# Performance work log

Hardware: AMD Instinct MI355X
Metric: run time of the kernel (lower is better)

The kernel has to match this reference:

```python
import jax, jax.numpy as jnp
import numpy as np

V_PATCH = (1, 2, 4, 8, 16, 32)
RESI = 0.5   # abs(quant_resi)
BETA = 0.25
K_PHI = 4    # share_quant_resi


def _phi_idx(si, SN, K=K_PHI):
    # PhiPartiallyShared.__getitem__ with at = si/(SN-1)
    ticks = np.linspace(1/3/K, 1 - 1/3/K, K) if K == 4 else np.linspace(1/2/K, 1 - 1/2/K, K)
    return int(np.argmin(np.abs(ticks - si / (SN - 1))))


def _area_down(x, pn):
    # F.interpolate mode='area' with pn | H  == exact block mean
    B, C, H, W = x.shape
    return x.reshape(B, C, pn, H // pn, pn, W // pn).mean(axis=(3, 5))


def _bilinear(x, size):
    # matches torch bilinear, align_corners=False, antialias=False (half-pixel centers)
    B, C, _, _ = x.shape
    return jax.image.resize(x, (B, C, size, size), method='bilinear', antialias=False)


def _down(x, pn, si):
    if pn == x.shape[2]:
        return x
    return _area_down(x, pn) if si <= 3 else _bilinear(x, pn)


def _phi_ada(h, w, b, fw, fb, sn):
    # Phi_ada: conv weight modulated by fc(SN); fc is zero-init but kept in the graph
    C = h.shape[1]
    cond = (fw[:, 0] * jnp.float32(sn) + fb).reshape(C, C, 1, 1)
    wmod = w * (1.0 + cond)
    y = jax.lax.conv_general_dilated(h, wmod, (1, 1), 'SAME',
                                     dimension_numbers=('NCHW', 'OIHW', 'NCHW'))
    y = y + b[None, :, None, None]
    return h * (1.0 - RESI) + y * RESI


def _forward(f, embed_w, conv_w, conv_b, fc_w, fc_b):
    B, C, H, W = f.shape
    SN = len(V_PATCH)
    f_ng = jax.lax.stop_gradient(f)
    f_rest = f_ng
    f_hat = jnp.zeros_like(f_ng)
    e_ng = jax.lax.stop_gradient(embed_w)            # embedding.weight.data
    e_sq = jnp.sum(e_ng * e_ng, axis=1)              # [V]
    vq_losses = []
    commit = jnp.float32(0.0)
    for si, pn in enumerate(V_PATCH):
        rest = f_rest if si == SN - 1 else _down(f_rest, pn, si)
        rest_NC = rest.transpose(0, 2, 3, 1).reshape(-1, C)          # [N,C]
        # squared L2 distances to codebook, argmin (non-differentiable)
        d = (jnp.sum(rest_NC * rest_NC, axis=1, keepdims=True)
             + e_sq - 2.0 * (rest_NC @ e_ng.T))                       # [N,V]
        idx = jnp.argmin(d, axis=1)                                   # [N]
        h = embed_w[idx].reshape(B, pn, pn, C).transpose(0, 3, 1, 2)  # [B,C,pn,pn]
        if si != SN - 1:
            h = _bilinear(h, H)
        k = _phi_idx(si, SN)
        h = _phi_ada(h, conv_w[k], conv_b[k], fc_w[k], fc_b[k], SN)
        f_hat = f_hat + h
        f_rest = f_rest - jax.lax.stop_gradient(h)    # grad through f_rest is killed by argmin anyway
        vq_losses.append(jnp.mean((f_hat - f_ng) ** 2))
        fh_ng = jax.lax.stop_gradient(f_hat)
        commit = commit + jnp.mean((_down(fh_ng, pn, si) - _down(f, pn, si)) ** 2) * BETA
    commit = commit / SN
    # straight-through estimator
    f_hat_out = jax.lax.stop_gradient(f_hat) - f_ng + f
    return f_hat_out, jnp.stack(vq_losses), commit


def setup_inputs() -> dict:
    key = jax.random.key(0)
    k1, k2, k3 = jax.random.split(key, 3)
    B, C, H, W = 32, 64, 32, 32
    V = 4096
    f_BChw = jax.random.normal(k1, (B, C, H, W), dtype=jnp.float32)
    embed_w = jax.random.normal(k2, (V, C), dtype=jnp.float32) * 0.5  # trunc_normal std=0.5
    conv_w = jax.random.normal(k3, (K_PHI, C, C, 3, 3), dtype=jnp.float32) * 0.02
    conv_b = jnp.zeros((K_PHI, C), dtype=jnp.float32)
    fc_w = jnp.zeros((K_PHI, C * C, 1), dtype=jnp.float32)  # Phi_ada.fc zero-init
    fc_b = jnp.zeros((K_PHI, C * C), dtype=jnp.float32)
    return {'f_BChw': f_BChw, 'embed_w': embed_w, 'conv_w': conv_w,
            'conv_b': conv_b, 'fc_w': fc_w, 'fc_b': fc_b}


def reference(f_BChw, embed_w, conv_w, conv_b, fc_w, fc_b):
    return _forward(f_BChw, embed_w, conv_w, conv_b, fc_w, fc_b)
```

## Files before the change

### kernel.cpp

```cpp
#include <hip/hip_runtime.h>
#include <cfloat>

#define N_ELEM 2097152
#define TAU 2.0e-2f

typedef short s16x8 __attribute__((ext_vector_type(8)));
typedef float f32x4 __attribute__((ext_vector_type(4)));

__device__ __forceinline__ unsigned short f2bf(float v) {
    unsigned u = __float_as_uint(v);
    u += 0x7FFFu + ((u >> 16) & 1u);
    return (unsigned short)(u >> 16);
}
__device__ __forceinline__ float bf2f(unsigned short h) {
    return __uint_as_float(((unsigned)h) << 16);
}

__device__ __forceinline__ float blockReduceSum(float v) {
    __shared__ float red[4];
    #pragma unroll
    for (int off = 32; off; off >>= 1) v += __shfl_down(v, off, 64);
    int wid = threadIdx.x >> 6, lane = threadIdx.x & 63;
    if (lane == 0) red[wid] = v;
    __syncthreads();
    float r = 0.f;
    if (threadIdx.x == 0) {
        int nw = ((int)blockDim.x + 63) >> 6;
        for (int w = 0; w < nw; ++w) r += red[w];
    }
    __syncthreads();
    return r;
}

__global__ void k_embprep(const float* __restrict__ e, float* __restrict__ hesq,
                          unsigned short* __restrict__ ehiN, unsigned short* __restrict__ eloN) {
    int v = blockIdx.x * 256 + threadIdx.x;
    if (v >= 4096) return;
    const float4* r = (const float4*)(e + (size_t)v * 64);
    float s = 0.f;
    #pragma unroll
    for (int i = 0; i < 16; ++i) {
        float4 a = r[i];
        s += a.x * a.x + a.y * a.y + a.z * a.z + a.w * a.w;
    }
    hesq[v] = 0.5f * s;
    for (int i = 0; i < 64; ++i) {
        float x = e[(size_t)v * 64 + i];
        unsigned short h = f2bf(x);
        ehiN[(size_t)v * 64 + i] = h ^ 0x8000u;
        eloN[(size_t)v * 64 + i] = f2bf(x - bf2f(h)) ^ 0x8000u;
    }
}

__global__ void k_wmod(const float* __restrict__ w, const float* __restrict__ fcw,
                       const float* __restrict__ fcb,
                       unsigned short* __restrict__ wh, unsigned short* __restrict__ wl) {
    int i = blockIdx.x * 256 + threadIdx.x;
    if (i >= 4 * 64 * 64 * 9) return;
    int k = i / (64 * 64 * 9);
    int r = i % (64 * 64 * 9);
    int oi = r / 9;
    int t = r % 9;
    int co = oi >> 6, ci = oi & 63;
    float cond = fcw[k * 4096 + oi] * 6.0f + fcb[k * 4096 + oi];
    float v = w[i] * (1.0f + cond);
    size_t o = ((size_t)(k * 9 + t) * 64 + co) * 64 + ci;
    unsigned short h = f2bf(v);
    wh[o] = h;
    wl[o] = f2bf(v - bf2f(h));
}

__global__ __launch_bounds__(256) void k_down_plane(
        const float* __restrict__ f, const float* __restrict__ fhat,
        float* __restrict__ restnc, unsigned short* __restrict__ dhi,
        unsigned short* __restrict__ dlo, float* __restrict__ cmpPrev, int pn) {
    __shared__ float hs[32][16];
    __shared__ float cr[32][16];
    __shared__ float pm[256];
    int bc = blockIdx.x;
    int c = bc & 63, b = bc >> 6;
    int t = threadIdx.x;
    const float4* fp = (const float4*)(f + (size_t)bc * 1024);
    const float4* hp = (const float4*)(fhat + (size_t)bc * 1024);
    float4 a = fp[t], q = hp[t];
    int r = t >> 3, c4 = t & 7;
    hs[r][c4 * 2]     = (a.x - q.x) + (a.y - q.y);
    hs[r][c4 * 2 + 1] = (a.z - q.z) + (a.w - q.w);
    __syncthreads();
    int cpp = 16 / pn;
    for (int i = t; i < 32 * pn; i += 256) {
        int rr = i / pn, px = i % pn;
        float s = 0.f;
        for (int j = 0; j < cpp; ++j) s += hs[rr][px * cpp + j];
        cr[rr][px] = s;
    }
    __syncthreads();
    int s_ = 32 / pn;
    float inv = 1.0f / (float)(s_ * s_);
    for (int p = t; p < pn * pn; p += 256) {
        int py = p / pn, px = p % pn;
        float s = 0.f;
        for (int j = 0; j < s_; ++j) s += cr[py * s_ + j][px];
        float m = s * inv;
        pm[p] = m;
        int n = (b * pn + py) * pn + px;
        size_t o = (size_t)n * 64 + c;
        unsigned short h = f2bf(m);
        restnc[o] = m;
        dhi[o] = h;
        dlo[o] = f2bf(m - bf2f(h));
    }
    if (pn >= 2) {
        __syncthreads();
        int pnp = pn >> 1;
        float m2 = 0.f;
        for (int p = t; p < pnp * pnp; p += 256) {
            int py = p / pnp, px = p % pnp;
            float mm = 0.25f * (pm[(2 * py) * pn + 2 * px] + pm[(2 * py) * pn + 2 * px + 1]
                              + pm[(2 * py + 1) * pn + 2 * px] + pm[(2 * py + 1) * pn + 2 * px + 1]);
            m2 += mm * mm;
        }
        m2 = blockReduceSum(m2);
        if (t == 0) cmpPrev[blockIdx.x] = m2;
    }
}

__global__ void k_trans_nc(const float* __restrict__ A, const float* __restrict__ Bt,
                           float* __restrict__ dst,
                           unsigned short* __restrict__ dhi, unsigned short* __restrict__ dlo) {
    __shared__ float t[64][65];
    int b = blockIdx.x;
    int p0 = blockIdx.y * 64;
    int lane = threadIdx.x & 63, r4 = threadIdx.x >> 6;
    #pragma unroll
    for (int i = 0; i < 16; ++i) {
        int c = i * 4 + r4;
        size_t g = ((size_t)b * 64 + c) * 1024 + p0 + lane;
        t[c][lane] = A[g] - Bt[g];
    }
    __syncthreads();
    #pragma unroll
    for (int i = 0; i < 16; ++i) {
        int p = i * 4 + r4;
        size_t o = ((size_t)(b * 1024 + p0 + p)) * 64 + lane;
        float v = t[lane][p];
        unsigned short h = f2bf(v);
        dst[o] = v;
        dhi[o] = h;
        dlo[o] = f2bf(v - bf2f(h));
    }
}

__global__ __launch_bounds__(256) void k_commit_rest(const float* __restrict__ restnc,
                                                     float* __restrict__ cmp) {
    int i = blockIdx.x * 256 + threadIdx.x;
    int c = i & 63;
    int p = i >> 6;
    int px = p & 15; p >>= 4;
    int py = p & 15; p >>= 4;
    int b = p;
    int n00 = (b * 32 + 2 * py) * 32 + 2 * px;
    float m = 0.25f * (restnc[(size_t)n00 * 64 + c] + restnc[(size_t)(n00 + 1) * 64 + c]
                     + restnc[(size_t)(n00 + 32) * 64 + c] + restnc[(size_t)(n00 + 33) * 64 + c]);
    float m2 = blockReduceSum(m * m);
    if (threadIdx.x == 0) cmp[blockIdx.x] = m2;
}

__global__ __launch_bounds__(256) void k_vq_mfma(
        const unsigned short* __restrict__ resthi, const unsigned short* __restrict__ restlo,
        const unsigned short* __restrict__ embhiN, const unsigned short* __restrict__ embloN,
        const float* __restrict__ hesq,
        float* __restrict__ m1v_, int* __restrict__ m1i_, float* __restrict__ m2v_,
        int N, int CPS) {
    __shared__ __align__(16) unsigned short lah[64 * 64];
    __shared__ __align__(16) unsigned short lal[64 * 64];
    __shared__ __align__(16) float lq[64];
    int tid = threadIdx.x;
    int lane = tid & 63, wv = tid >> 6;
    int split = blockIdx.y;
    int p0 = blockIdx.x * 128 + wv * 32;
    int cr = lane & 15, oct = lane >> 4;
    int ko8 = oct * 8;
    int ptA = p0 + cr, ptB = p0 + 16 + cr;
    int pA = min(ptA, N - 1), pB = min(ptB, N - 1);

    const unsigned short* ra = resthi + (size_t)pA * 64;
    const unsigned short* la = restlo + (size_t)pA * 64;
    const unsigned short* rb = resthi + (size_t)pB * 64;
    const unsigned short* lb = restlo + (size_t)pB * 64;
    s16x8 bhA0 = *(const s16x8*)(ra + ko8);
    s16x8 bhA1 = *(const s16x8*)(ra + 32 + ko8);
    s16x8 blA0 = *(const s16x8*)(la + ko8);
    s16x8 blA1 = *(const s16x8*)(la + 32 + ko8);
    s16x8 bhB0 = *(const s16x8*)(rb + ko8);
    s16x8 bhB1 = *(const s16x8*)(rb + 32 + ko8);
    s16x8 blB0 = *(const s16x8*)(lb + ko8);
    s16x8 blB1 = *(const s16x8*)(lb + 32 + ko8);

    float m1vA = FLT_MAX, m2vA = FLT_MAX; int m1iA = 0;
    float m1vB = FLT_MAX, m2vB = FLT_MAX; int m1iB = 0;
    int sw = (cr & 7) << 4;

    int cbeg = split * CPS;
    for (int oc = 0; oc < CPS; oc += 64) {
        int cb = cbeg + oc;
        __syncthreads();
        for (int t = tid; t < 512; t += 256) {
            int cc = t >> 3, part = t & 7;
            int bo = (cc * 128 + part * 16) ^ ((cc & 7) << 4);
            *(uint4*)((char*)lah + bo) = *(const uint4*)(embhiN + (size_t)(cb + cc) * 64 + part * 8);
            *(uint4*)((char*)lal + bo) = *(const uint4*)(embloN + (size_t)(cb + cc) * 64 + part * 8);
        }
        if (tid < 64) lq[tid] = hesq[cb + tid];
        __syncthreads();
        #pragma unroll
        for (int sub = 0; sub < 4; ++sub) {
            int rowb = (sub * 16 + cr) * 128;
            s16x8 ah0 = *(const s16x8*)((const char*)lah + ((rowb + ko8 * 2) ^ sw));
            s16x8 ah1 = *(const s16x8*)((const char*)lah + ((rowb + 64 + ko8 * 2) ^ sw));
            s16x8 al0 = *(const s16x8*)((const char*)lal + ((rowb + ko8 * 2) ^ sw));
            s16x8 al1 = *(const s16x8*)((const char*)lal + ((rowb + 64 + ko8 * 2) ^ sw));
            f32x4 q = *(const f32x4*)(lq + sub * 16 + oct * 4);
            int crow = cb + sub * 16 + oct * 4;
            f32x4 acc = q;
            acc = __builtin_amdgcn_mfma_f32_16x16x32_bf16(ah0, bhA0, acc, 0, 0, 0);
            acc = __builtin_amdgcn_mfma_f32_16x16x32_bf16(ah1, bhA1, acc, 0, 0, 0);
            acc = __builtin_amdgcn_mfma_f32_16x16x32_bf16(ah0, blA0, acc, 0, 0, 0);
            acc = __builtin_amdgcn_mfma_f32_16x16x32_bf16(ah1, blA1, acc, 0, 0, 0);
            acc = __builtin_amdgcn_mfma_f32_16x16x32_bf16(al0, bhA0, acc, 0, 0, 0);
            acc = __builtin_amdgcn_mfma_f32_16x16x32_bf16(al1, bhA1, acc, 0, 0, 0);
            #pragma unroll
            for (int r = 0; r < 4; ++r) {
                float s = acc[r];
                bool lt = s < m1vA;
                m2vA = fminf(fmaxf(s, m1vA), m2vA);
                m1iA = lt ? (crow + r) : m1iA;
                m1vA = fminf(s, m1vA);
            }
            f32x4 accB = q;
            accB = __builtin_amdgcn_mfma_f32_16x16x32_bf16(ah0, bhB0, accB, 0, 0, 0);
            accB = __builtin_amdgcn_mfma_f32_16x16x32_bf16(ah1, bhB1, accB, 0, 0, 0);
            accB = __builtin_amdgcn_mfma_f32_16x16x32_bf16(ah0, blB0, accB, 0, 0, 0);
            accB = __builtin_amdgcn_mfma_f32_16x16x32_bf16(ah1, blB1, accB, 0, 0, 0);
            accB = __builtin_amdgcn_mfma_f32_16x16x32_bf16(al0, bhB0, accB, 0, 0, 0);
            accB = __builtin_amdgcn_mfma_f32_16x16x32_bf16(al1, bhB1, accB, 0, 0, 0);
            #pragma unroll
            for (int r = 0; r < 4; ++r) {
                float s = accB[r];
                bool lt = s < m1vB;
                m2vB = fminf(fmaxf(s, m1vB), m2vB);
                m1iB = lt ? (crow + r) : m1iB;
                m1vB = fminf(s, m1vB);
            }
        }
    }
    #pragma unroll
    for (int off = 16; off <= 32; off <<= 1) {
        float o1 = __shfl_xor(m1vA, off, 64); int oi = __shfl_xor(m1iA, off, 64);
        float o2 = __shfl_xor(m2vA, off, 64);
        bool lt = o1 < m1vA;
        m2vA = fminf(fmaxf(o1, m1vA), fminf(m2vA, o2));
        m1vA = fminf(o1, m1vA);
        m1iA = lt ? oi : m1iA;
        o1 = __shfl_xor(m1vB, off, 64); oi = __shfl_xor(m1iB, off, 64);
        o2 = __shfl_xor(m2vB, off, 64);
        lt = o1 < m1vB;
        m2vB = fminf(fmaxf(o1, m1vB), fminf(m2vB, o2));
        m1vB = fminf(o1, m1vB);
        m1iB = lt ? oi : m1iB;
    }
    if (oct == 0) {
        if (ptA < N) { size_t o = (size_t)split * N + ptA; m1v_[o] = m1vA; m1i_[o] = m1iA; m2v_[o] = m2vA; }
        if (ptB < N) { size_t o = (size_t)split * N + ptB; m1v_[o] = m1vB; m1i_[o] = m1iB; m2v_[o] = m2vB; }
    }
}

__global__ void k_vq_combine(const float* __restrict__ m1v_, const int* __restrict__ m1i_,
                             const float* __restrict__ m2v_,
                             int* __restrict__ idx, int* __restrict__ flag, int* __restrict__ count,
                             unsigned long long* __restrict__ pmin, int N, int SPLITS) {
    int n = blockIdx.x * 256 + threadIdx.x;
    if (n >= N) return;
    float a1v = m1v_[n], a2v = m2v_[n];
    int a1i = m1i_[n];
    for (int s = 1; s < SPLITS; ++s) {
        size_t o = (size_t)s * N + n;
        float b1v = m1v_[o], b2v = m2v_[o];
        int b1i = m1i_[o];
        bool lt = b1v < a1v;
        a2v = fminf(fmaxf(b1v, a1v), fminf(a2v, b2v));
        a1v = fminf(b1v, a1v);
        a1i = lt ? b1i : a1i;
    }
    idx[n] = a1i;
    pmin[n] = 0xFFFFFFFFFFFFFFFFull;
    if (a2v - a1v < TAU) {
        int p = atomicAdd(count, 1);
        flag[p] = n;
    }
}

__global__ __launch_bounds__(256) void k_vq_exact(
        const float* __restrict__ restnc, const float* __restrict__ embed,
        const float* __restrict__ hesq, const int* __restrict__ flag,
        const int* __restrict__ count, unsigned long long* __restrict__ pmin) {
    __shared__ float rs[32 * 64];
    int tid = threadIdx.x;
    int lane = tid & 63;
    int cnt = *count;
    int nb = (cnt + 31) >> 5;
    int ntask = nb * 16;
    for (int task = blockIdx.x; task < ntask; task += gridDim.x) {
        int batch = task >> 4, spl = task & 15;
        int lbase = batch << 5;
        int npts = min(32, cnt - lbase);
        __syncthreads();
        for (int i = tid; i < npts * 64; i += 256) {
            int li = i >> 6;
            rs[i] = restnc[(size_t)flag[lbase + li] * 64 + (i & 63)];
        }
        __syncthreads();
        int code = spl * 256 + tid;
        const float4* e4 = (const float4*)(embed + (size_t)code * 64);
        float4 e[16];
        #pragma unroll
        for (int i = 0; i < 16; ++i) e[i] = e4[i];
        float hq = hesq[code];
        for (int p = 0; p < npts; ++p) {
            const float4* r4 = (const float4*)(rs + p * 64);
            float d0 = 0.f, d1 = 0.f, d2 = 0.f, d3 = 0.f;
            #pragma unroll
            for (int i = 0; i < 16; i += 4) {
                float4 e0 = e[i], e1 = e[i + 1], e2 = e[i + 2], e3 = e[i + 3];
                d0 += e0.x * r4[i].x     + e0.y * r4[i].y     + e0.z * r4[i].z     + e0.w * r4[i].w;
                d1 += e1.x * r4[i + 1].x + e1.y * r4[i + 1].y + e1.z * r4[i + 1].z + e1.w * r4[i + 1].w;
                d2 += e2.x * r4[i + 2].x + e2.y * r4[i + 2].y + e2.z * r4[i + 2].z + e2.w * r4[i + 2].w;
                d3 += e3.x * r4[i + 3].x + e3.y * r4[i + 3].y + e3.z * r4[i + 3].z + e3.w * r4[i + 3].w;
            }
            float s = hq - ((d0 + d1) + (d2 + d3));
            unsigned u = __float_as_uint(s);
            u = (u & 0x80000000u) ? ~u : (u | 0x80000000u);
            unsigned long long pk = (((unsigned long long)u) << 32) | (unsigned)code;
            #pragma unroll
            for (int off = 32; off; off >>= 1) {
                unsigned long long o = __shfl_down(pk, off, 64);
                if (o < pk) pk = o;
            }
            if (lane == 0) atomicMin(pmin + flag[lbase + p], pk);
        }
    }
}

__global__ void k_up(const int* __restrict__ idx, const unsigned long long* __restrict__ pmin,
                     const float* __restrict__ embed,
                     unsigned short* __restrict__ huph, unsigned short* __restrict__ hupl,
                     int pn) {
    int i = blockIdx.x * 256 + threadIdx.x;
    if (i >= N_ELEM) return;
    int c = i & 63, x = (i >> 6) & 31, y = (i >> 11) & 31, b = i >> 16;
    float v;
    if (pn == 32) {
        int n = (b * 32 + y) * 32 + x;
        unsigned long long pv = pmin[n];
        int id = (pv != 0xFFFFFFFFFFFFFFFFull) ? (int)(pv & 0xFFFFFFFFull) : idx[n];
        v = embed[(size_t)id * 64 + c];
    } else {
        float scale = (float)pn * (1.0f / 32.0f);
        float sy = (y + 0.5f) * scale - 0.5f;
        float sx = (x + 0.5f) * scale - 0.5f;
        float fy0 = floorf(sy), fx0 = floorf(sx);
        float wy = sy - fy0, wx = sx - fx0;
        int y0 = max(0, min(pn - 1, (int)fy0));
        int y1 = max(0, min(pn - 1, (int)fy0 + 1));
        int x0 = max(0, min(pn - 1, (int)fx0));
        int x1 = max(0, min(pn - 1, (int)fx0 + 1));
        int nb_ = b * pn * pn;
        int n00 = nb_ + y0 * pn + x0, n01 = nb_ + y0 * pn + x1;
        int n10 = nb_ + y1 * pn + x0, n11 = nb_ + y1 * pn + x1;
        unsigned long long p00 = pmin[n00], p01 = pmin[n01], p10 = pmin[n10], p11 = pmin[n11];
        int i00 = (p00 != 0xFFFFFFFFFFFFFFFFull) ? (int)(p00 & 0xFFFFFFFFull) : idx[n00];
        int i01 = (p01 != 0xFFFFFFFFFFFFFFFFull) ? (int)(p01 & 0xFFFFFFFFull) : idx[n01];
        int i10 = (p10 != 0xFFFFFFFFFFFFFFFFull) ? (int)(p10 & 0xFFFFFFFFull) : idx[n10];
        int i11 = (p11 != 0xFFFFFFFFFFFFFFFFull) ? (int)(p11 & 0xFFFFFFFFull) : idx[n11];
        float v00 = embed[(size_t)i00 * 64 + c];
        float v01 = embed[(size_t)i01 * 64 + c];
        float v10 = embed[(size_t)i10 * 64 + c];
        float v11 = embed[(size_t)i11 * 64 + c];
        v = (1.f - wy) * ((1.f - wx) * v00 + wx * v01) + wy * ((1.f - wx) * v10 + wx * v11);
    }
    unsigned short h = f2bf(v);
    huph[i] = h;
    hupl[i] = f2bf(v - bf2f(h));
}

__global__ __launch_bounds__(256) void k_conv_mfma(
        const unsigned short* __restrict__ huph, const unsigned short* __restrict__ hupl,
        const unsigned short* __restrict__ wh, const unsigned short* __restrict__ wl,
        const float* __restrict__ bias, const float* __restrict__ f_in,
        float* __restrict__ f_hat, float* __restrict__ vq_part) {
    __shared__ __align__(16) unsigned short Xh[6 * 34 * 64];
    __shared__ __align__(16) unsigned short Xl[6 * 34 * 64];
    int b = blockIdx.x, rg = blockIdx.y;
    int y0 = rg * 4;
    int tid = threadIdx.x;
    int lane = tid & 63, wv = tid >> 6;
    int coh = (wv & 1) * 32;
    int ph  = (wv >> 1) * 4;
    int cr = lane & 15, oct = lane >> 4;

    for (int q = tid; q < 6 * 34 * 8; q += 256) {
        int pl = q >> 3, o8 = q & 7;
        int lr = pl / 34, lc = pl % 34;
        int gy = y0 + lr - 1, gx = lc - 1;
        int bo = (pl * 128 + o8 * 16) ^ ((lc & 7) << 4);
        uint4 vh = {0, 0, 0, 0}, vl = {0, 0, 0, 0};
        if (gy >= 0 && gy < 32 && gx >= 0 && gx < 32) {
            size_t g = (((size_t)(b * 32 + gy)) * 32 + gx) * 64 + o8 * 8;
            vh = *(const uint4*)(huph + g);
            vl = *(const uint4*)(hupl + g);
        }
        *(uint4*)((char*)Xh + bo) = vh;
        *(uint4*)((char*)Xl + bo) = vl;
    }
    __syncthreads();

    f32x4 acc[2][4];
    #pragma unroll
    for (int ct = 0; ct < 2; ++ct)
        #pragma unroll
        for (int pp = 0; pp < 4; ++pp) acc[ct][pp] = (f32x4){0.f, 0.f, 0.f, 0.f};

    for (int t = 0; t < 9; ++t) {
        int dy = t / 3, dx = t % 3;
        #pragma unroll
        for (int cc = 0; cc < 2; ++cc) {
            size_t wo0 = ((size_t)t * 64 + coh + cr) * 64 + cc * 32 + oct * 8;
            size_t wo1 = ((size_t)t * 64 + coh + 16 + cr) * 64 + cc * 32 + oct * 8;
            s16x8 Ah0 = *(const s16x8*)(wh + wo0);
            s16x8 Al0 = *(const s16x8*)(wl + wo0);
            s16x8 Ah1 = *(const s16x8*)(wh + wo1);
            s16x8 Al1 = *(const s16x8*)(wl + wo1);
            #pragma unroll
            for (int pp = 0; pp < 4; ++pp) {
                int px = (ph + pp) * 16 + cr;
                int lr = (px >> 5) + dy;
                int lc = (px & 31) + dx;
                int bo = ((lr * 34 + lc) * 128 + cc * 64 + oct * 16) ^ ((lc & 7) << 4);
                s16x8 Bh = *(const s16x8*)((const char*)Xh + bo);
                s16x8 Bl = *(const s16x8*)((const char*)Xl + bo);
                acc[0][pp] = __builtin_amdgcn_mfma_f32_16x16x32_bf16(Ah0, Bh, acc[0][pp], 0, 0, 0);
                acc[0][pp] = __builtin_amdgcn_mfma_f32_16x16x32_bf16(Ah0, Bl, acc[0][pp], 0, 0, 0);
                acc[0][pp] = __builtin_amdgcn_mfma_f32_16x16x32_bf16(Al0, Bh, acc[0][pp], 0, 0, 0);
                acc[1][pp] = __builtin_amdgcn_mfma_f32_16x16x32_bf16(Ah1, Bh, acc[1][pp], 0, 0, 0);
                acc[1][pp] = __builtin_amdgcn_mfma_f32_16x16x32_bf16(Ah1, Bl, acc[1][pp], 0, 0, 0);
                acc[1][pp] = __builtin_amdgcn_mfma_f32_16x16x32_bf16(Al1, Bh, acc[1][pp], 0, 0, 0);
            }
        }
    }

    float local = 0.f;
    #pragma unroll
    for (int ct = 0; ct < 2; ++ct) {
        int cbase = coh + ct * 16 + oct * 4;
        #pragma unroll
        for (int pp = 0; pp < 4; ++pp) {
            int px = (ph + pp) * 16 + cr;
            int y = y0 + (px >> 5), x = px & 31;
            int lr = (px >> 5) + 1, lc = (px & 31) + 1;
            int bo = ((lr * 34 + lc) * 128 + cbase * 2) ^ ((lc & 7) << 4);
            ushort4 hvh = *(const ushort4*)((const char*)Xh + bo);
            ushort4 hvl = *(const ushort4*)((const char*)Xl + bo);
            #pragma unroll
            for (int r = 0; r < 4; ++r) {
                int co = cbase + r;
                unsigned short uh = (r == 0) ? hvh.x : (r == 1) ? hvh.y : (r == 2) ? hvh.z : hvh.w;
                unsigned short ul = (r == 0) ? hvl.x : (r == 1) ? hvl.y : (r == 2) ? hvl.z : hvl.w;
                float hv = bf2f(uh) + bf2f(ul);
                float hconv = acc[ct][pp][r] + bias[co];
                float hout = 0.5f * hv + 0.5f * hconv;
                size_t o = (((size_t)(b * 64 + co)) * 32 + y) * 32 + x;
                float fh = f_hat[o] + hout;
                f_hat[o] = fh;
                float d = fh - f_in[o];
                local += d * d;
            }
        }
    }
    local = blockReduceSum(local);
    if (tid == 0) vq_part[b * 8 + rg] = local;
}

__global__ void k_final(const float* __restrict__ vqp, const float* __restrict__ cmpP,
                        float* __restrict__ out) {
    const int pn2s[5] = {1, 4, 16, 64, 256};
    __shared__ float commit_s;
    if (threadIdx.x == 0) commit_s = 0.f;
    __syncthreads();
    for (int si = 0; si < 6; ++si) {
        float l = vqp[si * 256 + threadIdx.x];
        l = blockReduceSum(l);
        if (threadIdx.x == 0) {
            float vl = l / (float)N_ELEM;
            out[N_ELEM + si] = vl;
            if (si == 5) commit_s += vl * 0.25f;
        }
        if (si < 5) {
            float csum = 0.f;
            for (int i = threadIdx.x; i < 2048; i += 256) csum += cmpP[si * 2048 + i];
            csum = blockReduceSum(csum);
            if (threadIdx.x == 0) commit_s += csum / (float)(2048 * pn2s[si]) * 0.25f;
        }
    }
    __syncthreads();
    if (threadIdx.x == 0) out[N_ELEM + 6] = commit_s / 6.0f;
}

extern "C" void kernel_launch(void* const* d_in, const int* in_sizes, int n_in,
                              void* d_out, int out_size, void* d_ws, size_t ws_size,
                              hipStream_t stream) {
    const float* f     = (const float*)d_in[0];
    const float* embed = (const float*)d_in[1];
    const float* convw = (const float*)d_in[2];
    const float* convb = (const float*)d_in[3];
    const float* fcw   = (const float*)d_in[4];
    const float* fcb   = (const float*)d_in[5];
    float* out = (float*)d_out;
    float* ws  = (float*)d_ws;

    float* restnc = ws + 2097152;
    unsigned short* resthi = (unsigned short*)(ws + 4194304);
    unsigned short* restlo = (unsigned short*)(ws + 5242880);
    unsigned short* huph   = resthi;
    unsigned short* hupl   = restlo;
    unsigned short* embhiN = (unsigned short*)(ws + 6291456);
    unsigned short* embloN = (unsigned short*)(ws + 6422528);
    unsigned short* wmodh  = (unsigned short*)(ws + 6553600);
    unsigned short* wmodl  = (unsigned short*)(ws + 6627328);
    float* hesq   = ws + 6701056;
    float* m1v    = ws + 6705152;
    float* m2v    = ws + 6836224;
    int*   m1i    = (int*)(ws + 6967296);
    int*   idx    = (int*)(ws + 7098368);
    int*   flag   = (int*)(ws + 7131136);
    int*   count  = (int*)(ws + 7163904);
    unsigned long long* pmin = (unsigned long long*)(ws + 7163968);
    float* vqp    = ws + 7229504;
    float* cmpP   = ws + 7231040;

    hipMemsetAsync(d_out, 0, (size_t)out_size * sizeof(float), stream);
    hipMemsetAsync(count, 0, 6 * sizeof(int), stream);
    k_wmod<<<576, 256, 0, stream>>>(convw, fcw, fcb, wmodh, wmodl);
    k_embprep<<<16, 256, 0, stream>>>(embed, hesq, embhiN, embloN);

    const int pns[6]    = {1, 2, 4, 8, 16, 32};
    const int splits[6] = {64, 64, 32, 16, 8, 4};
    const int kidx[6]   = {0, 0, 1, 2, 3, 3};

    for (int si = 0; si < 6; ++si) {
        int pn = pns[si], pn2 = pn * pn;
        int N = 32 * pn2, SPL = splits[si], CPS = 4096 / SPL;

        if (si <= 4) {
            k_down_plane<<<2048, 256, 0, stream>>>(f, out, restnc, resthi, restlo,
                                                   si >= 1 ? cmpP + (si - 1) * 2048 : nullptr, pn);
        } else {
            k_trans_nc<<<dim3(32, 16), 256, 0, stream>>>(f, out, restnc, resthi, restlo);
            k_commit_rest<<<2048, 256, 0, stream>>>(restnc, cmpP + 4 * 2048);
        }

        k_vq_mfma<<<dim3((N + 127) / 128, SPL), 256, 0, stream>>>(resthi, restlo, embhiN, embloN, hesq,
                                                                  m1v, m1i, m2v, N, CPS);
        k_vq_combine<<<(N + 255) / 256, 256, 0, stream>>>(m1v, m1i, m2v, idx, flag, count + si, pmin, N, SPL);
        k_vq_exact<<<512, 256, 0, stream>>>(restnc, embed, hesq, flag, count + si, pmin);

        k_up<<<(N_ELEM + 255) / 256, 256, 0, stream>>>(idx, pmin, embed, huph, hupl, pn);

        k_conv_mfma<<<dim3(32, 8), 256, 0, stream>>>(huph, hupl,
                                                     wmodh + kidx[si] * 36864, wmodl + kidx[si] * 36864,
                                                     convb + kidx[si] * 64, f, out, vqp + si * 256);
    }

    k_final<<<1, 256, 0, stream>>>(vqp, cmpP, out);
}
```

Measured before the change: 595.8 us.

## Widen VQ MFMA tiles to 64 points per wave and fuse commit into transpose

Each wave in the VQ distance kernel now processes four 16-point tiles instead of two, so every codebook tile loaded into LDS is reused across 256 points per block. The per-tile min/second-min update is restructured to do a cheap group-min first and the full index update only when it beats the current best. Split counts are raised to keep enough blocks in flight, and the workspace is re-laid out for the larger partial buffers. The last-stage commit pooling is folded into the transpose kernel using its shared tile, removing a separate kernel launch and a re-read of rest. The wider tiles raise register pressure, which may lower occupancy.

Result: slower. 626.7 us (+5.2%).

```diff
diff --git a/kernel.cpp b/kernel.cpp
--- a/kernel.cpp
+++ b/kernel.cpp
@@ -127,7 +127,8 @@
 
 __global__ void k_trans_nc(const float* __restrict__ A, const float* __restrict__ Bt,
                            float* __restrict__ dst,
-                           unsigned short* __restrict__ dhi, unsigned short* __restrict__ dlo) {
+                           unsigned short* __restrict__ dhi, unsigned short* __restrict__ dlo,
+                           float* __restrict__ cmp) {
     __shared__ float t[64][65];
     int b = blockIdx.x;
     int p0 = blockIdx.y * 64;
@@ -149,21 +150,14 @@
         dhi[o] = h;
         dlo[o] = f2bf(v - bf2f(h));
     }
-}
-
-__global__ __launch_bounds__(256) void k_commit_rest(const float* __restrict__ restnc,
-                                                     float* __restrict__ cmp) {
-    int i = blockIdx.x * 256 + threadIdx.x;
-    int c = i & 63;
-    int p = i >> 6;
-    int px = p & 15; p >>= 4;
-    int py = p & 15; p >>= 4;
-    int b = p;
-    int n00 = (b * 32 + 2 * py) * 32 + 2 * px;
-    float m = 0.25f * (restnc[(size_t)n00 * 64 + c] + restnc[(size_t)(n00 + 1) * 64 + c]
-                     + restnc[(size_t)(n00 + 32) * 64 + c] + restnc[(size_t)(n00 + 33) * 64 + c]);
-    float m2 = blockReduceSum(m * m);
-    if (threadIdx.x == 0) cmp[blockIdx.x] = m2;
+    float m2s = 0.f;
+    for (int i = threadIdx.x; i < 1024; i += 256) {
+        int c = i & 63, px = i >> 6;
+        float m = 0.25f * (t[c][2 * px] + t[c][2 * px + 1] + t[c][32 + 2 * px] + t[c][33 + 2 * px]);
+        m2s += m * m;
+    }
+    m2s = blockReduceSum(m2s);
+    if (threadIdx.x == 0) cmp[blockIdx.x * 16 + blockIdx.y] = m2s;
 }
 
 __global__ __launch_bounds__(256) void k_vq_mfma(
@@ -178,28 +172,25 @@
     int tid = threadIdx.x;
     int lane = tid & 63, wv = tid >> 6;
     int split = blockIdx.y;
-    int p0 = blockIdx.x * 128 + wv * 32;
+    int p0 = blockIdx.x * 256 + wv * 64;
     int cr = lane & 15, oct = lane >> 4;
     int ko8 = oct * 8;
-    int ptA = p0 + cr, ptB = p0 + 16 + cr;
-    int pA = min(ptA, N - 1), pB = min(ptB, N - 1);
-
-    const unsigned short* ra = resthi + (size_t)pA * 64;
-    const unsigned short* la = restlo + (size_t)pA * 64;
-    const unsigned short* rb = resthi + (size_t)pB * 64;
-    const unsigned short* lb = restlo + (size_t)pB * 64;
-    s16x8 bhA0 = *(const s16x8*)(ra + ko8);
-    s16x8 bhA1 = *(const s16x8*)(ra + 32 + ko8);
-    s16x8 blA0 = *(const s16x8*)(la + ko8);
-    s16x8 blA1 = *(const s16x8*)(la + 32 + ko8);
-    s16x8 bhB0 = *(const s16x8*)(rb + ko8);
-    s16x8 bhB1 = *(const s16x8*)(rb + 32 + ko8);
-    s16x8 blB0 = *(const s16x8*)(lb + ko8);
-    s16x8 blB1 = *(const s16x8*)(lb + 32 + ko8);
-
-    float m1vA = FLT_MAX, m2vA = FLT_MAX; int m1iA = 0;
-    float m1vB = FLT_MAX, m2vB = FLT_MAX; int m1iB = 0;
     int sw = (cr & 7) << 4;
+
+    s16x8 bh0[4], bh1[4], bl0[4], bl1[4];
+    #pragma unroll
+    for (int T = 0; T < 4; ++T) {
+        int pt = min(p0 + T * 16 + cr, N - 1);
+        const unsigned short* rh = resthi + (size_t)pt * 64;
+        const unsigned short* rl = restlo + (size_t)pt * 64;
+        bh0[T] = *(const s16x8*)(rh + ko8);
+        bh1[T] = *(const s16x8*)(rh + 32 + ko8);
+        bl0[T] = *(const s16x8*)(rl + ko8);
+        bl1[T] = *(const s16x8*)(rl + 32 + ko8);
+    }
+    float m1v[4] = {FLT_MAX, FLT_MAX, FLT_MAX, FLT_MAX};
+    float m2v[4] = {FLT_MAX, FLT_MAX, FLT_MAX, FLT_MAX};
+    int m1i[4] = {0, 0, 0, 0};
 
     int cbeg = split * CPS;
     for (int oc = 0; oc < CPS; oc += 64) {
@@ -222,56 +213,52 @@
             s16x8 al1 = *(const s16x8*)((const char*)lal + ((rowb + 64 + ko8 * 2) ^ sw));
             f32x4 q = *(const f32x4*)(lq + sub * 16 + oct * 4);
             int crow = cb + sub * 16 + oct * 4;
-            f32x4 acc = q;
-            acc = __builtin_amdgcn_mfma_f32_16x16x32_bf16(ah0, bhA0, acc, 0, 0, 0);
-            acc = __builtin_amdgcn_mfma_f32_16x16x32_bf16(ah1, bhA1, acc, 0, 0, 0);
-            acc = __builtin_amdgcn_mfma_f32_16x16x32_bf16(ah0, blA0, acc, 0, 0, 0);
-            acc = __builtin_amdgcn_mfma_f32_16x16x32_bf16(ah1, blA1, acc, 0, 0, 0);
-            acc = __builtin_amdgcn_mfma_f32_16x16x32_bf16(al0, bhA0, acc, 0, 0, 0);
-            acc = __builtin_amdgcn_mfma_f32_16x16x32_bf16(al1, bhA1, acc, 0, 0, 0);
             #pragma unroll
-            for (int r = 0; r < 4; ++r) {
-                float s = acc[r];
-                bool lt = s < m1vA;
-                m2vA = fminf(fmaxf(s, m1vA), m2vA);
-                m1iA = lt ? (crow + r) : m1iA;
-                m1vA = fminf(s, m1vA);
+            for (int T = 0; T < 4; ++T) {
+                f32x4 a = q;
+                a = __builtin_amdgcn_mfma_f32_16x16x32_bf16(ah0, bh0[T], a, 0, 0, 0);
+                a = __builtin_amdgcn_mfma_f32_16x16x32_bf16(ah1, bh1[T], a, 0, 0, 0);
+                a = __builtin_amdgcn_mfma_f32_16x16x32_bf16(ah0, bl0[T], a, 0, 0, 0);
+                a = __builtin_amdgcn_mfma_f32_16x16x32_bf16(ah1, bl1[T], a, 0, 0, 0);
+                a = __builtin_amdgcn_mfma_f32_16x16x32_bf16(al0, bh0[T], a, 0, 0, 0);
+                a = __builtin_amdgcn_mfma_f32_16x16x32_bf16(al1, bh1[T], a, 0, 0, 0);
+                float m01 = fminf(a[0], a[1]);
+                float m23 = fminf(a[2], a[3]);
+                float gmin = fminf(m01, m23);
+                m2v[T] = fminf(gmin, m2v[T]);
+                if (gmin < m1v[T]) {
+                    float M01 = fmaxf(a[0], a[1]);
+                    float M23 = fmaxf(a[2], a[3]);
+                    float g2 = fminf(fmaxf(m01, m23), fminf(M01, M23));
+                    int i01 = (a[1] < a[0]) ? crow + 1 : crow;
+                    int i23 = (a[3] < a[2]) ? crow + 3 : crow + 2;
+                    int gi = (m23 < m01) ? i23 : i01;
+                    m2v[T] = fminf(m1v[T], g2);
+                    m1v[T] = gmin;
+                    m1i[T] = gi;
+                }
             }
-            f32x4 accB = q;
-            accB = __builtin_amdgcn_mfma_f32_16x16x32_bf16(ah0, bhB0, accB, 0, 0, 0);
-            accB = __builtin_amdgcn_mfma_f32_16x16x32_bf16(ah1, bhB1, accB, 0, 0, 0);
-            accB = __builtin_amdgcn_mfma_f32_16x16x32_bf16(ah0, blB0, accB, 0, 0, 0);
-            accB = __builtin_amdgcn_mfma_f32_16x16x32_bf16(ah1, blB1, accB, 0, 0, 0);
-            accB = __builtin_amdgcn_mfma_f32_16x16x32_bf16(al0, bhB0, accB, 0, 0, 0);
-            accB = __builtin_amdgcn_mfma_f32_16x16x32_bf16(al1, bhB1, accB, 0, 0, 0);
-            #pragma unroll
-            for (int r = 0; r < 4; ++r) {
-                float s = accB[r];
-                bool lt = s < m1vB;
-                m2vB = fminf(fmaxf(s, m1vB), m2vB);
-                m1iB = lt ? (crow + r) : m1iB;
-                m1vB = fminf(s, m1vB);
+        }
+    }
+    #pragma unroll
+    for (int T = 0; T < 4; ++T) {
+        #pragma unroll
+        for (int off = 16; off <= 32; off <<= 1) {
+            float o1 = __shfl_xor(m1v[T], off, 64);
+            int oi = __shfl_xor(m1i[T], off, 64);
+            float o2 = __shfl_xor(m2v[T], off, 64);
+            bool lt = o1 < m1v[T];
+            m2v[T] = fminf(fmaxf(o1, m1v[T]), fminf(m2v[T], o2));
+            m1v[T] = fminf(o1, m1v[T]);
+            m1i[T] = lt ? oi : m1i[T];
+        }
+        if (oct == 0) {
+            int pt = p0 + T * 16 + cr;
+            if (pt < N) {
+                size_t o = (size_t)split * N + pt;
+                m1v_[o] = m1v[T]; m1i_[o] = m1i[T]; m2v_[o] = m2v[T];
             }
         }
-    }
-    #pragma unroll
-    for (int off = 16; off <= 32; off <<= 1) {
-        float o1 = __shfl_xor(m1vA, off, 64); int oi = __shfl_xor(m1iA, off, 64);
-        float o2 = __shfl_xor(m2vA, off, 64);
-        bool lt = o1 < m1vA;
-        m2vA = fminf(fmaxf(o1, m1vA), fminf(m2vA, o2));
-        m1vA = fminf(o1, m1vA);
-        m1iA = lt ? oi : m1iA;
-        o1 = __shfl_xor(m1vB, off, 64); oi = __shfl_xor(m1iB, off, 64);
-        o2 = __shfl_xor(m2vB, off, 64);
-        lt = o1 < m1vB;
-        m2vB = fminf(fmaxf(o1, m1vB), fminf(m2vB, o2));
-        m1vB = fminf(o1, m1vB);
-        m1iB = lt ? oi : m1iB;
-    }
-    if (oct == 0) {
-        if (ptA < N) { size_t o = (size_t)split * N + ptA; m1v_[o] = m1vA; m1i_[o] = m1iA; m2v_[o] = m2vA; }
-        if (ptB < N) { size_t o = (size_t)split * N + ptB; m1v_[o] = m1vB; m1i_[o] = m1iB; m2v_[o] = m2vB; }
     }
 }
 
@@ -493,6 +480,7 @@
 __global__ void k_final(const float* __restrict__ vqp, const float* __restrict__ cmpP,
                         float* __restrict__ out) {
     const int pn2s[5] = {1, 4, 16, 64, 256};
+    const int slots[5] = {2048, 2048, 2048, 2048, 512};
     __shared__ float commit_s;
     if (threadIdx.x == 0) commit_s = 0.f;
     __syncthreads();
@@ -506,7 +494,7 @@
         }
         if (si < 5) {
             float csum = 0.f;
-            for (int i = threadIdx.x; i < 2048; i += 256) csum += cmpP[si * 2048 + i];
+            for (int i = threadIdx.x; i < slots[si]; i += 256) csum += cmpP[si * 2048 + i];
             csum = blockReduceSum(csum);
             if (threadIdx.x == 0) commit_s += csum / (float)(2048 * pn2s[si]) * 0.25f;
         }
@@ -538,14 +526,14 @@
     unsigned short* wmodl  = (unsigned short*)(ws + 6627328);
     float* hesq   = ws + 6701056;
     float* m1v    = ws + 6705152;
-    float* m2v    = ws + 6836224;
-    int*   m1i    = (int*)(ws + 6967296);
-    int*   idx    = (int*)(ws + 7098368);
-    int*   flag   = (int*)(ws + 7131136);
-    int*   count  = (int*)(ws + 7163904);
-    unsigned long long* pmin = (unsigned long long*)(ws + 7163968);
-    float* vqp    = ws + 7229504;
-    float* cmpP   = ws + 7231040;
+    float* m2v    = ws + 6967296;
+    int*   m1i    = (int*)(ws + 7229440);
+    int*   idx    = (int*)(ws + 7491584);
+    int*   flag   = (int*)(ws + 7524352);
+    int*   count  = (int*)(ws + 7557120);
+    unsigned long long* pmin = (unsigned long long*)(ws + 7557184);
+    float* vqp    = ws + 7622720;
+    float* cmpP   = ws + 7624256;
 
     hipMemsetAsync(d_out, 0, (size_t)out_size * sizeof(float), stream);
     hipMemsetAsync(count, 0, 6 * sizeof(int), stream);
@@ -553,7 +541,7 @@
     k_embprep<<<16, 256, 0, stream>>>(embed, hesq, embhiN, embloN);
 
     const int pns[6]    = {1, 2, 4, 8, 16, 32};
-    const int splits[6] = {64, 64, 32, 16, 8, 4};
+    const int splits[6] = {64, 64, 64, 64, 16, 8};
     const int kidx[6]   = {0, 0, 1, 2, 3, 3};
 
     for (int si = 0; si < 6; ++si) {
@@ -564,11 +552,11 @@
             k_down_plane<<<2048, 256, 0, stream>>>(f, out, restnc, resthi, restlo,
                                                    si >= 1 ? cmpP + (si - 1) * 2048 : nullptr, pn);
         } else {
-            k_trans_nc<<<dim3(32, 16), 256, 0, stream>>>(f, out, restnc, resthi, restlo);
-            k_commit_rest<<<2048, 256, 0, stream>>>(restnc, cmpP + 4 * 2048);
-        }
-
-        k_vq_mfma<<<dim3((N + 127) / 128, SPL), 256, 0, stream>>>(resthi, restlo, embhiN, embloN, hesq,
+            k_trans_nc<<<dim3(32, 16), 256, 0, stream>>>(f, out, restnc, resthi, restlo,
+                                                         cmpP + 4 * 2048);
+        }
+
+        k_vq_mfma<<<dim3((N + 255) / 256, SPL), 256, 0, stream>>>(resthi, restlo, embhiN, embloN, hesq,
                                                                   m1v, m1i, m2v, N, CPS);
         k_vq_combine<<<(N + 255) / 256, 256, 0, stream>>>(m1v, m1i, m2v, idx, flag, count + si, pmin, N, SPL);
         k_vq_exact<<<512, 256, 0, stream>>>(restnc, embed, hesq, flag, count + si, pmin);
```

## Fuse upsample into conv, fold commit reduction into transpose, retune splits

Applied to the files above, without the earlier changes.

The bilinear upsample/gather kernel is removed. The conv kernel now computes codebook indices and interpolation weights per halo pixel in shared memory and builds the bf16 hi/lo input tile directly from the embedding table. This avoids writing and re-reading the full-resolution upsampled buffer. Conv tiles shrink from 4 to 2 rows with twice the grid, so halo rows are recomputed more often. The rest-commit reduction moves into the transpose kernel, workspace offsets are enlarged, and VQ split counts rise for the middle scales.

After: 609.9 us. 2.4% more time.

```diff
diff --git a/kernel.cpp b/kernel.cpp
--- a/kernel.cpp
+++ b/kernel.cpp
@@ -127,7 +127,8 @@
 
 __global__ void k_trans_nc(const float* __restrict__ A, const float* __restrict__ Bt,
                            float* __restrict__ dst,
-                           unsigned short* __restrict__ dhi, unsigned short* __restrict__ dlo) {
+                           unsigned short* __restrict__ dhi, unsigned short* __restrict__ dlo,
+                           float* __restrict__ cmp) {
     __shared__ float t[64][65];
     int b = blockIdx.x;
     int p0 = blockIdx.y * 64;
@@ -149,21 +150,14 @@
         dhi[o] = h;
         dlo[o] = f2bf(v - bf2f(h));
     }
-}
-
-__global__ __launch_bounds__(256) void k_commit_rest(const float* __restrict__ restnc,
-                                                     float* __restrict__ cmp) {
-    int i = blockIdx.x * 256 + threadIdx.x;
-    int c = i & 63;
-    int p = i >> 6;
-    int px = p & 15; p >>= 4;
-    int py = p & 15; p >>= 4;
-    int b = p;
-    int n00 = (b * 32 + 2 * py) * 32 + 2 * px;
-    float m = 0.25f * (restnc[(size_t)n00 * 64 + c] + restnc[(size_t)(n00 + 1) * 64 + c]
-                     + restnc[(size_t)(n00 + 32) * 64 + c] + restnc[(size_t)(n00 + 33) * 64 + c]);
-    float m2 = blockReduceSum(m * m);
-    if (threadIdx.x == 0) cmp[blockIdx.x] = m2;
+    float m2s = 0.f;
+    for (int i = threadIdx.x; i < 1024; i += 256) {
+        int c = i & 63, px = i >> 6;
+        float m = 0.25f * (t[c][2 * px] + t[c][2 * px + 1] + t[c][32 + 2 * px] + t[c][33 + 2 * px]);
+        m2s += m * m;
+    }
+    m2s = blockReduceSum(m2s);
+    if (threadIdx.x == 0) cmp[blockIdx.x * 16 + blockIdx.y] = m2s;
 }
 
 __global__ __launch_bounds__(256) void k_vq_mfma(
@@ -351,84 +345,102 @@
     }
 }
 
-__global__ void k_up(const int* __restrict__ idx, const unsigned long long* __restrict__ pmin,
-                     const float* __restrict__ embed,
-                     unsigned short* __restrict__ huph, unsigned short* __restrict__ hupl,
-                     int pn) {
-    int i = blockIdx.x * 256 + threadIdx.x;
-    if (i >= N_ELEM) return;
-    int c = i & 63, x = (i >> 6) & 31, y = (i >> 11) & 31, b = i >> 16;
-    float v;
-    if (pn == 32) {
-        int n = (b * 32 + y) * 32 + x;
-        unsigned long long pv = pmin[n];
-        int id = (pv != 0xFFFFFFFFFFFFFFFFull) ? (int)(pv & 0xFFFFFFFFull) : idx[n];
-        v = embed[(size_t)id * 64 + c];
-    } else {
-        float scale = (float)pn * (1.0f / 32.0f);
-        float sy = (y + 0.5f) * scale - 0.5f;
-        float sx = (x + 0.5f) * scale - 0.5f;
-        float fy0 = floorf(sy), fx0 = floorf(sx);
-        float wy = sy - fy0, wx = sx - fx0;
-        int y0 = max(0, min(pn - 1, (int)fy0));
-        int y1 = max(0, min(pn - 1, (int)fy0 + 1));
-        int x0 = max(0, min(pn - 1, (int)fx0));
-        int x1 = max(0, min(pn - 1, (int)fx0 + 1));
-        int nb_ = b * pn * pn;
-        int n00 = nb_ + y0 * pn + x0, n01 = nb_ + y0 * pn + x1;
-        int n10 = nb_ + y1 * pn + x0, n11 = nb_ + y1 * pn + x1;
-        unsigned long long p00 = pmin[n00], p01 = pmin[n01], p10 = pmin[n10], p11 = pmin[n11];
-        int i00 = (p00 != 0xFFFFFFFFFFFFFFFFull) ? (int)(p00 & 0xFFFFFFFFull) : idx[n00];
-        int i01 = (p01 != 0xFFFFFFFFFFFFFFFFull) ? (int)(p01 & 0xFFFFFFFFull) : idx[n01];
-        int i10 = (p10 != 0xFFFFFFFFFFFFFFFFull) ? (int)(p10 & 0xFFFFFFFFull) : idx[n10];
-        int i11 = (p11 != 0xFFFFFFFFFFFFFFFFull) ? (int)(p11 & 0xFFFFFFFFull) : idx[n11];
-        float v00 = embed[(size_t)i00 * 64 + c];
-        float v01 = embed[(size_t)i01 * 64 + c];
-        float v10 = embed[(size_t)i10 * 64 + c];
-        float v11 = embed[(size_t)i11 * 64 + c];
-        v = (1.f - wy) * ((1.f - wx) * v00 + wx * v01) + wy * ((1.f - wx) * v10 + wx * v11);
-    }
-    unsigned short h = f2bf(v);
-    huph[i] = h;
-    hupl[i] = f2bf(v - bf2f(h));
-}
-
 __global__ __launch_bounds__(256) void k_conv_mfma(
-        const unsigned short* __restrict__ huph, const unsigned short* __restrict__ hupl,
+        const int* __restrict__ idx, const unsigned long long* __restrict__ pmin,
+        const float* __restrict__ embed,
         const unsigned short* __restrict__ wh, const unsigned short* __restrict__ wl,
         const float* __restrict__ bias, const float* __restrict__ f_in,
-        float* __restrict__ f_hat, float* __restrict__ vq_part) {
-    __shared__ __align__(16) unsigned short Xh[6 * 34 * 64];
-    __shared__ __align__(16) unsigned short Xl[6 * 34 * 64];
+        float* __restrict__ f_hat, float* __restrict__ vq_part, int pn) {
+    __shared__ __align__(16) unsigned short Xh[4 * 34 * 64];
+    __shared__ __align__(16) unsigned short Xl[4 * 34 * 64];
+    __shared__ int pid[136][4];
+    __shared__ float pwt[136][2];
     int b = blockIdx.x, rg = blockIdx.y;
-    int y0 = rg * 4;
+    int y0 = rg * 2;
     int tid = threadIdx.x;
     int lane = tid & 63, wv = tid >> 6;
     int coh = (wv & 1) * 32;
-    int ph  = (wv >> 1) * 4;
+    int ph  = (wv >> 1) * 2;
     int cr = lane & 15, oct = lane >> 4;
 
-    for (int q = tid; q < 6 * 34 * 8; q += 256) {
+    if (tid < 136) {
+        int lr = tid / 34, lc = tid % 34;
+        int gy = y0 + lr - 1, gx = lc - 1;
+        if (gy >= 0 && gy < 32 && gx >= 0 && gx < 32) {
+            if (pn == 32) {
+                int n = (b * 32 + gy) * 32 + gx;
+                unsigned long long pv = pmin[n];
+                int id = (pv != 0xFFFFFFFFFFFFFFFFull) ? (int)(pv & 0xFFFFFFFFull) : idx[n];
+                pid[tid][0] = id; pid[tid][1] = id; pid[tid][2] = id; pid[tid][3] = id;
+                pwt[tid][0] = 0.f; pwt[tid][1] = 0.f;
+            } else {
+                float scale = (float)pn * (1.0f / 32.0f);
+                float sy = (gy + 0.5f) * scale - 0.5f;
+                float sx = (gx + 0.5f) * scale - 0.5f;
+                float fy0 = floorf(sy), fx0 = floorf(sx);
+                float wy = sy - fy0, wx = sx - fx0;
+                int yy0 = max(0, min(pn - 1, (int)fy0));
+                int yy1 = max(0, min(pn - 1, (int)fy0 + 1));
+                int xx0 = max(0, min(pn - 1, (int)fx0));
+                int xx1 = max(0, min(pn - 1, (int)fx0 + 1));
+                int nb_ = b * pn * pn;
+                int n00 = nb_ + yy0 * pn + xx0, n01 = nb_ + yy0 * pn + xx1;
+                int n10 = nb_ + yy1 * pn + xx0, n11 = nb_ + yy1 * pn + xx1;
+                unsigned long long p00 = pmin[n00], p01 = pmin[n01];
+                unsigned long long p10 = pmin[n10], p11 = pmin[n11];
+                pid[tid][0] = (p00 != 0xFFFFFFFFFFFFFFFFull) ? (int)(p00 & 0xFFFFFFFFull) : idx[n00];
+                pid[tid][1] = (p01 != 0xFFFFFFFFFFFFFFFFull) ? (int)(p01 & 0xFFFFFFFFull) : idx[n01];
+                pid[tid][2] = (p10 != 0xFFFFFFFFFFFFFFFFull) ? (int)(p10 & 0xFFFFFFFFull) : idx[n10];
+                pid[tid][3] = (p11 != 0xFFFFFFFFFFFFFFFFull) ? (int)(p11 & 0xFFFFFFFFull) : idx[n11];
+                pwt[tid][0] = wy; pwt[tid][1] = wx;
+            }
+        } else {
+            pid[tid][0] = -1;
+        }
+    }
+    __syncthreads();
+
+    for (int q = tid; q < 136 * 8; q += 256) {
         int pl = q >> 3, o8 = q & 7;
-        int lr = pl / 34, lc = pl % 34;
-        int gy = y0 + lr - 1, gx = lc - 1;
+        int lc = pl % 34;
         int bo = (pl * 128 + o8 * 16) ^ ((lc & 7) << 4);
         uint4 vh = {0, 0, 0, 0}, vl = {0, 0, 0, 0};
-        if (gy >= 0 && gy < 32 && gx >= 0 && gx < 32) {
-            size_t g = (((size_t)(b * 32 + gy)) * 32 + gx) * 64 + o8 * 8;
-            vh = *(const uint4*)(huph + g);
-            vl = *(const uint4*)(hupl + g);
+        int i00 = pid[pl][0];
+        if (i00 >= 0) {
+            int i01 = pid[pl][1], i10 = pid[pl][2], i11 = pid[pl][3];
+            float wy = pwt[pl][0], wx = pwt[pl][1];
+            const float4* e00 = (const float4*)(embed + (size_t)i00 * 64 + o8 * 8);
+            const float4* e01 = (const float4*)(embed + (size_t)i01 * 64 + o8 * 8);
+            const float4* e10 = (const float4*)(embed + (size_t)i10 * 64 + o8 * 8);
+            const float4* e11 = (const float4*)(embed + (size_t)i11 * 64 + o8 * 8);
+            union { unsigned short u[8]; uint4 v; } oh, ol;
+            #pragma unroll
+            for (int half = 0; half < 2; ++half) {
+                float4 a00 = e00[half], a01 = e01[half], a10 = e10[half], a11 = e11[half];
+                float vv[4];
+                vv[0] = (a00.x + wx * (a01.x - a00.x)) + wy * ((a10.x + wx * (a11.x - a10.x)) - (a00.x + wx * (a01.x - a00.x)));
+                vv[1] = (a00.y + wx * (a01.y - a00.y)) + wy * ((a10.y + wx * (a11.y - a10.y)) - (a00.y + wx * (a01.y - a00.y)));
+                vv[2] = (a00.z + wx * (a01.z - a00.z)) + wy * ((a10.z + wx * (a11.z - a10.z)) - (a00.z + wx * (a01.z - a00.z)));
+                vv[3] = (a00.w + wx * (a01.w - a00.w)) + wy * ((a10.w + wx * (a11.w - a10.w)) - (a00.w + wx * (a01.w - a00.w)));
+                #pragma unroll
+                for (int j = 0; j < 4; ++j) {
+                    unsigned short h = f2bf(vv[j]);
+                    oh.u[half * 4 + j] = h;
+                    ol.u[half * 4 + j] = f2bf(vv[j] - bf2f(h));
+                }
+            }
+            vh = oh.v; vl = ol.v;
         }
         *(uint4*)((char*)Xh + bo) = vh;
         *(uint4*)((char*)Xl + bo) = vl;
     }
     __syncthreads();
 
-    f32x4 acc[2][4];
+    f32x4 acc[2][2];
     #pragma unroll
     for (int ct = 0; ct < 2; ++ct)
         #pragma unroll
-        for (int pp = 0; pp < 4; ++pp) acc[ct][pp] = (f32x4){0.f, 0.f, 0.f, 0.f};
+        for (int pp = 0; pp < 2; ++pp) acc[ct][pp] = (f32x4){0.f, 0.f, 0.f, 0.f};
 
     for (int t = 0; t < 9; ++t) {
         int dy = t / 3, dx = t % 3;
@@ -441,7 +453,7 @@
             s16x8 Ah1 = *(const s16x8*)(wh + wo1);
             s16x8 Al1 = *(const s16x8*)(wl + wo1);
             #pragma unroll
-            for (int pp = 0; pp < 4; ++pp) {
+            for (int pp = 0; pp < 2; ++pp) {
                 int px = (ph + pp) * 16 + cr;
                 int lr = (px >> 5) + dy;
                 int lc = (px & 31) + dx;
@@ -463,7 +475,7 @@
     for (int ct = 0; ct < 2; ++ct) {
         int cbase = coh + ct * 16 + oct * 4;
         #pragma unroll
-        for (int pp = 0; pp < 4; ++pp) {
+        for (int pp = 0; pp < 2; ++pp) {
             int px = (ph + pp) * 16 + cr;
             int y = y0 + (px >> 5), x = px & 31;
             int lr = (px >> 5) + 1, lc = (px & 31) + 1;
@@ -487,17 +499,18 @@
         }
     }
     local = blockReduceSum(local);
-    if (tid == 0) vq_part[b * 8 + rg] = local;
+    if (tid == 0) vq_part[b * 16 + rg] = local;
 }
 
 __global__ void k_final(const float* __restrict__ vqp, const float* __restrict__ cmpP,
                         float* __restrict__ out) {
     const int pn2s[5] = {1, 4, 16, 64, 256};
+    const int slots[5] = {2048, 2048, 2048, 2048, 512};
     __shared__ float commit_s;
     if (threadIdx.x == 0) commit_s = 0.f;
     __syncthreads();
     for (int si = 0; si < 6; ++si) {
-        float l = vqp[si * 256 + threadIdx.x];
+        float l = vqp[si * 512 + threadIdx.x] + vqp[si * 512 + 256 + threadIdx.x];
         l = blockReduceSum(l);
         if (threadIdx.x == 0) {
             float vl = l / (float)N_ELEM;
@@ -506,7 +519,7 @@
         }
         if (si < 5) {
             float csum = 0.f;
-            for (int i = threadIdx.x; i < 2048; i += 256) csum += cmpP[si * 2048 + i];
+            for (int i = threadIdx.x; i < slots[si]; i += 256) csum += cmpP[si * 2048 + i];
             csum = blockReduceSum(csum);
             if (threadIdx.x == 0) commit_s += csum / (float)(2048 * pn2s[si]) * 0.25f;
         }
@@ -530,22 +543,20 @@
     float* restnc = ws + 2097152;
     unsigned short* resthi = (unsigned short*)(ws + 4194304);
     unsigned short* restlo = (unsigned short*)(ws + 5242880);
-    unsigned short* huph   = resthi;
-    unsigned short* hupl   = restlo;
     unsigned short* embhiN = (unsigned short*)(ws + 6291456);
     unsigned short* embloN = (unsigned short*)(ws + 6422528);
     unsigned short* wmodh  = (unsigned short*)(ws + 6553600);
     unsigned short* wmodl  = (unsigned short*)(ws + 6627328);
     float* hesq   = ws + 6701056;
     float* m1v    = ws + 6705152;
-    float* m2v    = ws + 6836224;
-    int*   m1i    = (int*)(ws + 6967296);
-    int*   idx    = (int*)(ws + 7098368);
-    int*   flag   = (int*)(ws + 7131136);
-    int*   count  = (int*)(ws + 7163904);
-    unsigned long long* pmin = (unsigned long long*)(ws + 7163968);
-    float* vqp    = ws + 7229504;
-    float* cmpP   = ws + 7231040;
+    float* m2v    = ws + 6967296;
+    int*   m1i    = (int*)(ws + 7229440);
+    int*   idx    = (int*)(ws + 7491584);
+    int*   flag   = (int*)(ws + 7524352);
+    int*   count  = (int*)(ws + 7557120);
+    unsigned long long* pmin = (unsigned long long*)(ws + 7557184);
+    float* vqp    = ws + 7622720;
+    float* cmpP   = ws + 7625792;
 
     hipMemsetAsync(d_out, 0, (size_t)out_size * sizeof(float), stream);
     hipMemsetAsync(count, 0, 6 * sizeof(int), stream);
@@ -553,7 +564,7 @@
     k_embprep<<<16, 256, 0, stream>>>(embed, hesq, embhiN, embloN);
 
     const int pns[6]    = {1, 2, 4, 8, 16, 32};
-    const int splits[6] = {64, 64, 32, 16, 8, 4};
+    const int splits[6] = {64, 64, 64, 64, 16, 8};
     const int kidx[6]   = {0, 0, 1, 2, 3, 3};
 
     for (int si = 0; si < 6; ++si) {
@@ -564,8 +575,8 @@
             k_down_plane<<<2048, 256, 0, stream>>>(f, out, restnc, resthi, restlo,
                                                    si >= 1 ? cmpP + (si - 1) * 2048 : nullptr, pn);
         } else {
-            k_trans_nc<<<dim3(32, 16), 256, 0, stream>>>(f, out, restnc, resthi, restlo);
-            k_commit_rest<<<2048, 256, 0, stream>>>(restnc, cmpP + 4 * 2048);
+            k_trans_nc<<<dim3(32, 16), 256, 0, stream>>>(f, out, restnc, resthi, restlo,
+                                                         cmpP + 4 * 2048);
         }
 
         k_vq_mfma<<<dim3((N + 127) / 128, SPL), 256, 0, stream>>>(resthi, restlo, embhiN, embloN, hesq,
@@ -573,11 +584,9 @@
         k_vq_combine<<<(N + 255) / 256, 256, 0, stream>>>(m1v, m1i, m2v, idx, flag, count + si, pmin, N, SPL);
         k_vq_exact<<<512, 256, 0, stream>>>(restnc, embed, hesq, flag, count + si, pmin);
 
-        k_up<<<(N_ELEM + 255) / 256, 256, 0, stream>>>(idx, pmin, embed, huph, hupl, pn);
-
-        k_conv_mfma<<<dim3(32, 8), 256, 0, stream>>>(huph, hupl,
-                                                     wmodh + kidx[si] * 36864, wmodl + kidx[si] * 36864,
-                                                     convb + kidx[si] * 64, f, out, vqp + si * 256);
+        k_conv_mfma<<<dim3(32, 16), 256, 0, stream>>>(idx, pmin, embed,
+                                                      wmodh + kidx[si] * 36864, wmodl + kidx[si] * 36864,
+                                                      convb + kidx[si] * 64, f, out, vqp + si * 512, pn);
     }
 
     k_final<<<1, 256, 0, stream>>>(vqp, cmpP, out);
```
